# Performance work log

Measured on AMD Instinct MI355X. Metric: run time of the kernel, lower is better.

The kernel has to match this reference:

```python
import jax, jax.numpy as jnp
import numpy as np

B, N, T, F = 8, 5000, 24, 10
H = 128
HEADS = 4
HORIZON = 6
E = 80000
NEG_SLOPE = 0.2


def setup_inputs() -> dict:
    key = jax.random.key(0)
    ks = jax.random.split(key, 24)
    s = 0.1
    inp = {
        'x': jax.random.normal(ks[0], (B, N, T, F), jnp.float32),
        'w_ih0': jax.random.normal(ks[1], (3 * H, F), jnp.float32) * s,
        'w_hh0': jax.random.normal(ks[2], (3 * H, H), jnp.float32) * s,
        'b_ih0': jax.random.normal(ks[3], (3 * H,), jnp.float32) * s,
        'b_hh0': jax.random.normal(ks[4], (3 * H,), jnp.float32) * s,
        'w_ih1': jax.random.normal(ks[5], (3 * H, H), jnp.float32) * s,
        'w_hh1': jax.random.normal(ks[6], (3 * H, H), jnp.float32) * s,
        'b_ih1': jax.random.normal(ks[7], (3 * H,), jnp.float32) * s,
        'b_hh1': jax.random.normal(ks[8], (3 * H,), jnp.float32) * s,
        'gat1_w': jax.random.normal(ks[9], (HEADS * H, H), jnp.float32) * s,
        'gat1_asrc': jax.random.normal(ks[10], (HEADS, H), jnp.float32) * s,
        'gat1_adst': jax.random.normal(ks[11], (HEADS, H), jnp.float32) * s,
        'gat1_b': jax.random.normal(ks[12], (H,), jnp.float32) * s,
        'gat2_w': jax.random.normal(ks[13], (HEADS * H, H), jnp.float32) * s,
        'gat2_asrc': jax.random.normal(ks[14], (HEADS, H), jnp.float32) * s,
        'gat2_adst': jax.random.normal(ks[15], (HEADS, H), jnp.float32) * s,
        'gat2_b': jax.random.normal(ks[16], (H,), jnp.float32) * s,
        'fc_w': jax.random.normal(ks[17], (HORIZON, H), jnp.float32) * s,
        'fc_b': jax.random.normal(ks[18], (HORIZON,), jnp.float32) * s,
        'edge_index': jax.random.randint(ks[19], (2, E), 0, N, jnp.int64),
    }
    return inp


def _gru_layer(xs, w_ih, w_hh, b_ih, b_hh):
    # xs: [BN, T, Fin] -> outputs [BN, T, H] (PyTorch GRU gate order r,z,n)
    gi = jnp.einsum('btf,gf->btg', xs, w_ih) + b_ih  # [BN, T, 3H]
    h0 = jnp.zeros((xs.shape[0], H), xs.dtype)

    def step(h, gi_t):
        gh = h @ w_hh.T + b_hh
        i_r, i_z, i_n = jnp.split(gi_t, 3, axis=-1)
        h_r, h_z, h_n = jnp.split(gh, 3, axis=-1)
        r = jax.nn.sigmoid(i_r + h_r)
        z = jax.nn.sigmoid(i_z + h_z)
        n = jnp.tanh(i_n + r * h_n)
        h_new = (1.0 - z) * n + z * h
        return h_new, h_new

    _, hs = jax.lax.scan(step, h0, jnp.swapaxes(gi, 0, 1))
    return jnp.swapaxes(hs, 0, 1)


def _gat(h, src, dst, W, a_src, a_dst, b, num_nodes):
    # PyG GATConv, heads=4, concat=False (mean), self-loops already in src/dst
    wh = (h @ W.T).reshape(num_nodes, HEADS, H)          # [BN, heads, H]
    alpha_s = jnp.sum(wh * a_src[None], axis=-1)          # [BN, heads]
    alpha_d = jnp.sum(wh * a_dst[None], axis=-1)
    e = jax.nn.leaky_relu(alpha_s[src] + alpha_d[dst], NEG_SLOPE)  # [Eb, heads]
    emax = jax.ops.segment_max(e, dst, num_segments=num_nodes)
    emax = jnp.where(jnp.isfinite(emax), emax, 0.0)
    ex = jnp.exp(e - emax[dst])
    denom = jax.ops.segment_sum(ex, dst, num_segments=num_nodes)
    alpha = ex / (denom[dst] + 1e-16)                     # segment softmax over incoming edges
    out = jax.ops.segment_sum(alpha[..., None] * wh[src], dst, num_segments=num_nodes)
    return out.mean(axis=1) + b


def _batched_edges(edge_index):
    offsets = (jnp.arange(B, dtype=edge_index.dtype) * N)[:, None]
    src = (edge_index[0][None, :] + offsets).reshape(-1)
    dst = (edge_index[1][None, :] + offsets).reshape(-1)
    loops = jnp.arange(B * N, dtype=edge_index.dtype)     # PyG add_self_loops=True
    return jnp.concatenate([src, loops]), jnp.concatenate([dst, loops])


def reference(x, w_ih0, w_hh0, b_ih0, b_hh0, w_ih1, w_hh1, b_ih1, b_hh1,
              gat1_w, gat1_asrc, gat1_adst, gat1_b,
              gat2_w, gat2_asrc, gat2_adst, gat2_b,
              fc_w, fc_b, edge_index):
    src, dst = _batched_edges(edge_index)
    xs = x.reshape(B * N, T, F)
    h1 = _gru_layer(xs, w_ih0, w_hh0, b_ih0, b_hh0)
    h2 = _gru_layer(h1, w_ih1, w_hh1, b_ih1, b_hh1)
    temporal = h2[:, -1, :]                               # [B*N, H]
    s = jax.nn.relu(_gat(temporal, src, dst, gat1_w, gat1_asrc, gat1_adst, gat1_b, B * N))
    s = jax.nn.relu(_gat(s, src, dst, gat2_w, gat2_asrc, gat2_adst, gat2_b, B * N))
    out = s @ fc_w.T + fc_b
    return out.reshape(B, N, HORIZON)
```

## Files before the change

kernel.cpp:

```cpp
#include <hip/hip_runtime.h>
#include <math.h>

#define T_STEPS 24
#define F_IN 10
#define HDIM 128
#define E_EDGES 80000
#define B_BATCH 8
#define N_NODES 5000
#define BN_TOTAL 40000
#define BE 640000
#define NE 680000

typedef __attribute__((ext_vector_type(8))) short s16x8;
typedef __attribute__((ext_vector_type(4))) short s16x4;
typedef __attribute__((ext_vector_type(4))) float fx4;
typedef __attribute__((ext_vector_type(2))) float fx2;
typedef __attribute__((ext_vector_type(4))) unsigned int ux4;
typedef __attribute__((ext_vector_type(2))) unsigned int ux2;

__device__ __forceinline__ float rcpf_(float v) { return __builtin_amdgcn_rcpf(v); }
__device__ __forceinline__ float sigmoidf_(float v) { return rcpf_(1.f + __expf(-v)); }
__device__ __forceinline__ float tanhf_(float v) { float e = __expf(2.f * v); return 1.f - 2.f * rcpf_(e + 1.f); }

__device__ __forceinline__ short f2b(float f) {
    unsigned u = __float_as_uint(f);
    unsigned r = (u + 0x7fffu + ((u >> 16) & 1u)) >> 16;
    return (short)r;
}
__device__ __forceinline__ unsigned int pkbf(float a, float b) {
    unsigned int r;
    asm("v_cvt_pk_bf16_f32 %0, %1, %2" : "=v"(r) : "v"(a), "v"(b));
    return r;
}
__device__ __forceinline__ float bfu(unsigned short u) {
    return __uint_as_float(((unsigned)u) << 16);
}

#define VMW0 asm volatile("s_waitcnt vmcnt(0)" ::: "memory")

__global__ void pack_w(const float* __restrict__ wih0, const float* __restrict__ whh0,
                       const float* __restrict__ wih1, const float* __restrict__ whh1,
                       const float* __restrict__ g1w, const float* __restrict__ g2w,
                       short* __restrict__ pk) {
    int id = blockIdx.x * 256 + threadIdx.x;
    if (id >= 290816) return;
    if (id < 147456) {
        int mat = id / 49152, r = id % 49152;
        int nf = r / 2048, r2 = r % 2048, kf = r2 / 512, r3 = r2 % 512, lane = r3 / 8, j = r3 % 8;
        int n = nf * 16 + (lane & 15), k = kf * 32 + (lane >> 4) * 8 + j;
        const float* src = (mat == 0) ? whh0 : (mat == 1) ? whh1 : wih1;
        pk[id] = f2b(src[n * 128 + k]);
    } else if (id < 159744) {
        int r = id - 147456;
        int nf = r / 512, r2 = r % 512, lane = r2 / 8, j = r2 % 8;
        int n = nf * 16 + (lane & 15), k = (lane >> 4) * 8 + j;
        pk[id] = (k < F_IN) ? f2b(wih0[n * F_IN + k]) : (short)0;
    } else {
        const float* src = (id < 225280) ? g1w : g2w;
        int r = (id < 225280) ? (id - 159744) : (id - 225280);
        int nf = r / 2048, r2 = r % 2048, kf = r2 / 512, r3 = r2 % 512, lane = r3 / 8, j = r3 % 8;
        int n = nf * 16 + (lane & 15), k = kf * 32 + (lane >> 4) * 8 + j;
        pk[id] = f2b(src[n * 128 + k]);
    }
}

__global__ __launch_bounds__(512, 1) void gru_mfma(
    const float* __restrict__ x, const short* __restrict__ pk,
    const float* __restrict__ bih0, const float* __restrict__ bhh0,
    const float* __restrict__ bih1, const float* __restrict__ bhh1,
    float* __restrict__ temporal) {
    __shared__ __align__(16) short h1b[64 * 128];
    __shared__ __align__(16) short h2b[64 * 128];
    __shared__ __align__(16) short ih1s[49152];
    __shared__ __align__(16) short ih0s[12288];
    __shared__ __align__(16) float blds[2][4][128];
    const int tid = threadIdx.x;
    const int w = tid >> 6, l = tid & 63;
    const int lm = l & 15, lk = l >> 4;
    const int jb = w * 16 + lk * 4;
    const long sb = (long)blockIdx.x * 64;

    {
        const char* src1 = (const char*)(pk + 98304);
#pragma unroll
        for (int r = 0; r < 12; ++r) {
            const int off = (w * 12 + r) * 1024;
            __builtin_amdgcn_global_load_lds(
                (const __attribute__((address_space(1))) unsigned int*)(src1 + off + l * 16),
                (__attribute__((address_space(3))) unsigned int*)((char*)ih1s + off), 16, 0, 0);
        }
        const char* src0 = (const char*)(pk + 147456);
#pragma unroll
        for (int r = 0; r < 3; ++r) {
            const int off = (w * 3 + r) * 1024;
            __builtin_amdgcn_global_load_lds(
                (const __attribute__((address_space(1))) unsigned int*)(src0 + off + l * 16),
                (__attribute__((address_space(3))) unsigned int*)((char*)ih0s + off), 16, 0, 0);
        }
    }
    if (tid < 128) {
        const int j = tid;
        blds[0][0][j] = bih0[j] + bhh0[j];
        blds[0][1][j] = bih0[128 + j] + bhh0[128 + j];
        blds[0][2][j] = bhh0[256 + j];
        blds[0][3][j] = bih0[256 + j];
    } else if (tid < 256) {
        const int j = tid - 128;
        blds[1][0][j] = bih1[j] + bhh1[j];
        blds[1][1][j] = bih1[128 + j] + bhh1[128 + j];
        blds[1][2][j] = bhh1[256 + j];
        blds[1][3][j] = bih1[256 + j];
    }
    for (int i = tid; i < 64 * 128; i += 512) { h1b[i] = 0; h2b[i] = 0; }

    s16x8 whh0r[3][4], whh1r[3][4];
#pragma unroll
    for (int g = 0; g < 3; ++g)
#pragma unroll
        for (int kf = 0; kf < 4; ++kf) {
            const int idx = ((((g * 8 + w) * 4) + kf) * 64 + l) * 8;
            whh0r[g][kf] = *(const s16x8*)&pk[idx];
            whh1r[g][kf] = *(const s16x8*)&pk[49152 + idx];
        }

    fx4 h1s[4], h2s[4];
#pragma unroll
    for (int mf = 0; mf < 4; ++mf) { h1s[mf] = (fx4)(0.f); h2s[mf] = (fx4)(0.f); }

    VMW0;
    __syncthreads();

    for (int tt = 0; tt < T_STEPS; ++tt) {
        ux4 xu[4];
#pragma unroll
        for (int mf = 0; mf < 4; ++mf) {
            fx2 a0 = (fx2)(0.f), a1 = (fx2)(0.f), a2 = (fx2)(0.f), a3 = (fx2)(0.f);
            const float* xr = x + (sb + mf * 16 + lm) * (T_STEPS * F_IN) + tt * F_IN;
            if (lk == 0) {
                a0 = *(const fx2*)(xr);     a1 = *(const fx2*)(xr + 2);
                a2 = *(const fx2*)(xr + 4); a3 = *(const fx2*)(xr + 6);
            } else if (lk == 1) {
                a0 = *(const fx2*)(xr + 8);
            }
            ux4 t = { pkbf(a0.x, a0.y), pkbf(a1.x, a1.y), pkbf(a2.x, a2.y), pkbf(a3.x, a3.y) };
            xu[mf] = t;
        }
        fx4 acc[4][4];
#pragma unroll
        for (int p = 0; p < 4; ++p) {
            const fx4 bv = *(const fx4*)&blds[0][p][jb];
#pragma unroll
            for (int mf = 0; mf < 4; ++mf) acc[p][mf] = bv;
        }
#pragma unroll
        for (int kf = 0; kf < 4; ++kf) {
            s16x8 bfr[4];
#pragma unroll
            for (int mf = 0; mf < 4; ++mf) {
                const int m = mf * 16 + lm;
                const int slot = (kf * 4 + lk) ^ (m & 7);
                bfr[mf] = *(const s16x8*)&h1b[m * 128 + slot * 8];
            }
#pragma unroll
            for (int g = 0; g < 3; ++g) {
                const int part = (g == 2) ? 2 : g;
#pragma unroll
                for (int mf = 0; mf < 4; ++mf)
                    acc[part][mf] = __builtin_amdgcn_mfma_f32_16x16x32_bf16(whh0r[g][kf], bfr[mf], acc[part][mf], 0, 0, 0);
            }
        }
#pragma unroll
        for (int g = 0; g < 3; ++g) {
            const int part = (g == 2) ? 3 : g;
            const s16x8 af = *(const s16x8*)&ih0s[((g * 8 + w) * 64 + l) * 8];
#pragma unroll
            for (int mf = 0; mf < 4; ++mf)
                acc[part][mf] = __builtin_amdgcn_mfma_f32_16x16x32_bf16(af, __builtin_bit_cast(s16x8, xu[mf]), acc[part][mf], 0, 0, 0);
        }
        ux2 w1[4];
#pragma unroll
        for (int mf = 0; mf < 4; ++mf) {
#pragma unroll
            for (int rg = 0; rg < 4; ++rg) {
                const float r = sigmoidf_(acc[0][mf][rg]);
                const float z = sigmoidf_(acc[1][mf][rg]);
                const float n = tanhf_(acc[3][mf][rg] + r * acc[2][mf][rg]);
                h1s[mf][rg] = n + z * (h1s[mf][rg] - n);
            }
            ux2 q = { pkbf(h1s[mf][0], h1s[mf][1]), pkbf(h1s[mf][2], h1s[mf][3]) };
            w1[mf] = q;
        }
#pragma unroll
        for (int p = 0; p < 4; ++p) {
            const fx4 bv = *(const fx4*)&blds[1][p][jb];
#pragma unroll
            for (int mf = 0; mf < 4; ++mf) acc[p][mf] = bv;
        }
#pragma unroll
        for (int kf = 0; kf < 4; ++kf) {
            s16x8 bfr[4];
#pragma unroll
            for (int mf = 0; mf < 4; ++mf) {
                const int m = mf * 16 + lm;
                const int slot = (kf * 4 + lk) ^ (m & 7);
                bfr[mf] = *(const s16x8*)&h2b[m * 128 + slot * 8];
            }
#pragma unroll
            for (int g = 0; g < 3; ++g) {
                const int part = (g == 2) ? 2 : g;
#pragma unroll
                for (int mf = 0; mf < 4; ++mf)
                    acc[part][mf] = __builtin_amdgcn_mfma_f32_16x16x32_bf16(whh1r[g][kf], bfr[mf], acc[part][mf], 0, 0, 0);
            }
        }
        __syncthreads();
#pragma unroll
        for (int mf = 0; mf < 4; ++mf) {
            const int m = mf * 16 + lm;
            const int slot = (jb >> 3) ^ (m & 7);
            *(ux2*)&h1b[m * 128 + slot * 8 + (jb & 7)] = w1[mf];
        }
        __syncthreads();
#pragma unroll
        for (int kf = 0; kf < 4; ++kf) {
            s16x8 bfr[4];
#pragma unroll
            for (int mf = 0; mf < 4; ++mf) {
                const int m = mf * 16 + lm;
                const int slot = (kf * 4 + lk) ^ (m & 7);
                bfr[mf] = *(const s16x8*)&h1b[m * 128 + slot * 8];
            }
#pragma unroll
            for (int g = 0; g < 3; ++g) {
                const int part = (g == 2) ? 3 : g;
                const s16x8 af = *(const s16x8*)&ih1s[((((g * 8 + w) * 4) + kf) * 64 + l) * 8];
#pragma unroll
                for (int mf = 0; mf < 4; ++mf)
                    acc[part][mf] = __builtin_amdgcn_mfma_f32_16x16x32_bf16(af, bfr[mf], acc[part][mf], 0, 0, 0);
            }
        }
#pragma unroll
        for (int mf = 0; mf < 4; ++mf) {
#pragma unroll
            for (int rg = 0; rg < 4; ++rg) {
                const float r = sigmoidf_(acc[0][mf][rg]);
                const float z = sigmoidf_(acc[1][mf][rg]);
                const float n = tanhf_(acc[3][mf][rg] + r * acc[2][mf][rg]);
                h2s[mf][rg] = n + z * (h2s[mf][rg] - n);
            }
            const int m = mf * 16 + lm;
            const int slot = (jb >> 3) ^ (m & 7);
            ux2 q = { pkbf(h2s[mf][0], h2s[mf][1]), pkbf(h2s[mf][2], h2s[mf][3]) };
            *(ux2*)&h2b[m * 128 + slot * 8 + (jb & 7)] = q;
        }
        __syncthreads();
    }
#pragma unroll
    for (int mf = 0; mf < 4; ++mf) {
        const long m = sb + mf * 16 + lm;
        *(fx4*)&temporal[m * 128 + jb] = h2s[mf];
    }
}

__global__ void csr_count(const int* __restrict__ edge1, int* __restrict__ cnt) {
    int e = blockIdx.x * 256 + threadIdx.x;
    if (e >= NE) return;
    int d;
    if (e < BE) { int b = e / E_EDGES; d = edge1[e - b * E_EDGES] + b * N_NODES; }
    else d = e - BE;
    atomicAdd(&cnt[d], 1);
}

__global__ void csr_scan(const int* cnt, int* offs, int* curs) {
    __shared__ int part[1024];
    const int t = threadIdx.x;
    const int base = t * 40;
    int end = base + 40; if (end > BN_TOTAL) end = BN_TOTAL;
    int s = 0;
    for (int i = base; i < end; ++i) s += cnt[i];
    part[t] = s;
    __syncthreads();
    for (int off = 1; off < 1024; off <<= 1) {
        int v = (t >= off) ? part[t - off] : 0;
        __syncthreads();
        part[t] += v;
        __syncthreads();
    }
    int run = part[t] - s;
    for (int i = base; i < end; ++i) {
        int c = cnt[i];
        offs[i] = run; curs[i] = run; run += c;
    }
    if (t == 1023) offs[BN_TOTAL] = NE;
}

__global__ void csr_fill(const int* __restrict__ edge1, int* __restrict__ curs, int* __restrict__ esort) {
    int e = blockIdx.x * 256 + threadIdx.x;
    if (e >= NE) return;
    int d;
    if (e < BE) { int b = e / E_EDGES; d = edge1[e - b * E_EDGES] + b * N_NODES; }
    else d = e - BE;
    int pos = atomicAdd(&curs[d], 1);
    esort[pos] = e;
}

__global__ __launch_bounds__(256, 2) void gat_gemm(const float* __restrict__ feat,
                                                   const short* __restrict__ pkg,
                                                   const float* __restrict__ asrc,
                                                   const float* __restrict__ adst,
                                                   unsigned short* __restrict__ whb,
                                                   float* __restrict__ AS, float* __restrict__ AD) {
    __shared__ __align__(16) short fb[128 * 128];
    __shared__ float reda[4][128];
    __shared__ float redb[4][128];
    const int tid = threadIdx.x;
    const int w = tid >> 6, l = tid & 63;
    const int lm = l & 15, lk = l >> 4;
    const int i0 = blockIdx.x * 128;
    const int j0 = blockIdx.y * 128;
#pragma unroll
    for (int it = 0; it < 16; ++it) {
        const int idx = it * 256 + tid;
        const int r = idx >> 5, kq = idx & 31;
        fx4 v = (fx4)(0.f);
        const int row = i0 + r;
        if (row < BN_TOTAL) v = *(const fx4*)&feat[(size_t)row * 128 + kq * 4];
        const int slot = (kq >> 1) ^ (r & 7);
        ux2 pv = { pkbf(v.x, v.y), pkbf(v.z, v.w) };
        *(ux2*)&fb[r * 128 + slot * 8 + (kq & 1) * 4] = pv;
    }
    __syncthreads();
    fx4 acc[2][8];
#pragma unroll
    for (int jf = 0; jf < 2; ++jf)
#pragma unroll
        for (int mf = 0; mf < 8; ++mf) acc[jf][mf] = (fx4)(0.f);
#pragma unroll
    for (int kf = 0; kf < 4; ++kf) {
        s16x8 bfr[8];
#pragma unroll
        for (int mf = 0; mf < 8; ++mf) {
            const int m = mf * 16 + lm;
            const int slot = (kf * 4 + lk) ^ (m & 7);
            bfr[mf] = *(const s16x8*)&fb[m * 128 + slot * 8];
        }
#pragma unroll
        for (int jf = 0; jf < 2; ++jf) {
            const int nf = (j0 >> 4) + w * 2 + jf;
            const s16x8 af = *(const s16x8*)&pkg[((nf * 4 + kf) * 64 + l) * 8];
#pragma unroll
            for (int mf = 0; mf < 8; ++mf)
                acc[jf][mf] = __builtin_amdgcn_mfma_f32_16x16x32_bf16(af, bfr[mf], acc[jf][mf], 0, 0, 0);
        }
    }
    float ps[8], pd[8];
#pragma unroll
    for (int mf = 0; mf < 8; ++mf) { ps[mf] = 0.f; pd[mf] = 0.f; }
#pragma unroll
    for (int jf = 0; jf < 2; ++jf) {
        const int cb = w * 32 + jf * 16 + lk * 4;
        const fx4 s4 = *(const fx4*)&asrc[j0 + cb];
        const fx4 d4 = *(const fx4*)&adst[j0 + cb];
        const int nb = j0 + cb;
#pragma unroll
        for (int mf = 0; mf < 8; ++mf) {
            const int m = i0 + mf * 16 + lm;
            const fx4 a = acc[jf][mf];
            if (m < BN_TOTAL) {
                ux2 pv = { pkbf(a.x, a.y), pkbf(a.z, a.w) };
                *(ux2*)&whb[(size_t)m * 512 + nb] = pv;
            }
            ps[mf] += a.x * s4.x + a.y * s4.y + a.z * s4.z + a.w * s4.w;
            pd[mf] += a.x * d4.x + a.y * d4.y + a.z * d4.z + a.w * d4.w;
        }
    }
#pragma unroll
    for (int off = 16; off <= 32; off <<= 1) {
#pragma unroll
        for (int mf = 0; mf < 8; ++mf) {
            ps[mf] += __shfl_xor(ps[mf], off);
            pd[mf] += __shfl_xor(pd[mf], off);
        }
    }
    if (lk == 0) {
#pragma unroll
        for (int mf = 0; mf < 8; ++mf) {
            reda[w][mf * 16 + lm] = ps[mf];
            redb[w][mf * 16 + lm] = pd[mf];
        }
    }
    __syncthreads();
    if (tid < 128) {
        const int row = i0 + tid;
        if (row < BN_TOTAL) {
            const float a = reda[0][tid] + reda[1][tid] + reda[2][tid] + reda[3][tid];
            const float b = redb[0][tid] + redb[1][tid] + redb[2][tid] + redb[3][tid];
            AS[row * 4 + (j0 >> 7)] = a;
            AD[row * 4 + (j0 >> 7)] = b;
        }
    }
}

__device__ __forceinline__ int decode_src(int eid, const int* __restrict__ edge0) {
    if (eid < BE) { int b = eid / E_EDGES; return edge0[eid - b * E_EDGES] + b * N_NODES; }
    return eid - BE;
}

__global__ __launch_bounds__(256) void gat_aggregate(const unsigned short* __restrict__ whb,
                                                     const float* __restrict__ AS, const float* __restrict__ AD,
                                                     const int* __restrict__ offs, const int* __restrict__ esort,
                                                     const int* __restrict__ edge0, const float* __restrict__ bias,
                                                     float* __restrict__ outf,
                                                     const float* __restrict__ fcw, const float* __restrict__ fcb,
                                                     float* __restrict__ out6) {
    const int lane = threadIdx.x & 63;
    const int bid = blockIdx.x;
    const int d = (bid & 7) * N_NODES + (bid >> 3) * 4 + (threadIdx.x >> 6);
    const int e0 = offs[d], e1 = offs[d + 1];
    const fx4 ad4 = *(const fx4*)&AD[d * 4];
    float mx0 = -1e30f, mx1 = -1e30f, mx2 = -1e30f, mx3 = -1e30f;
    float den0 = 0.f, den1 = 0.f, den2 = 0.f, den3 = 0.f;
    float acc[8] = {0.f, 0.f, 0.f, 0.f, 0.f, 0.f, 0.f, 0.f};
    for (int e = e0; e < e1; ++e) {
        const int src = decode_src(esort[e], edge0);
        const fx4 as4 = *(const fx4*)&AS[src * 4];
        float v0 = as4.x + ad4.x; v0 = v0 > 0.f ? v0 : 0.2f * v0;
        float v1 = as4.y + ad4.y; v1 = v1 > 0.f ? v1 : 0.2f * v1;
        float v2 = as4.z + ad4.z; v2 = v2 > 0.f ? v2 : 0.2f * v2;
        float v3 = as4.w + ad4.w; v3 = v3 > 0.f ? v3 : 0.2f * v3;
        const float n0 = fmaxf(mx0, v0), n1 = fmaxf(mx1, v1), n2 = fmaxf(mx2, v2), n3 = fmaxf(mx3, v3);
        const float c0 = __expf(mx0 - n0), c1 = __expf(mx1 - n1), c2 = __expf(mx2 - n2), c3 = __expf(mx3 - n3);
        const float ex0 = __expf(v0 - n0), ex1 = __expf(v1 - n1), ex2 = __expf(v2 - n2), ex3 = __expf(v3 - n3);
        mx0 = n0; mx1 = n1; mx2 = n2; mx3 = n3;
        den0 = den0 * c0 + ex0; den1 = den1 * c1 + ex1;
        den2 = den2 * c2 + ex2; den3 = den3 * c3 + ex3;
        const unsigned int* wr = (const unsigned int*)(whb + (size_t)src * 512);
        const unsigned int u0 = wr[lane];
        const unsigned int u1 = wr[64 + lane];
        const unsigned int u2 = wr[128 + lane];
        const unsigned int u3 = wr[192 + lane];
        acc[0] = acc[0] * c0 + ex0 * bfu((unsigned short)u0);
        acc[1] = acc[1] * c0 + ex0 * bfu((unsigned short)(u0 >> 16));
        acc[2] = acc[2] * c1 + ex1 * bfu((unsigned short)u1);
        acc[3] = acc[3] * c1 + ex1 * bfu((unsigned short)(u1 >> 16));
        acc[4] = acc[4] * c2 + ex2 * bfu((unsigned short)u2);
        acc[5] = acc[5] * c2 + ex2 * bfu((unsigned short)(u2 >> 16));
        acc[6] = acc[6] * c3 + ex3 * bfu((unsigned short)u3);
        acc[7] = acc[7] * c3 + ex3 * bfu((unsigned short)(u3 >> 16));
    }
    const float i0v = rcpf_(den0 + 1e-16f), i1v = rcpf_(den1 + 1e-16f);
    const float i2v = rcpf_(den2 + 1e-16f), i3v = rcpf_(den3 + 1e-16f);
    const int c0i = 2 * lane, c1i = 2 * lane + 1;
    const float o0r = 0.25f * (acc[0] * i0v + acc[2] * i1v + acc[4] * i2v + acc[6] * i3v) + bias[c0i];
    const float o1r = 0.25f * (acc[1] * i0v + acc[3] * i1v + acc[5] * i2v + acc[7] * i3v) + bias[c1i];
    const float o0 = fmaxf(o0r, 0.f);
    const float o1 = fmaxf(o1r, 0.f);
    if (fcw == nullptr) {
        fx2 ov = { o0, o1 };
        *(fx2*)&outf[(size_t)d * 128 + c0i] = ov;
    } else {
        float p[6];
#pragma unroll
        for (int m = 0; m < 6; ++m) p[m] = o0 * fcw[m * 128 + c0i] + o1 * fcw[m * 128 + c1i];
#pragma unroll
        for (int off = 32; off > 0; off >>= 1) {
#pragma unroll
            for (int m = 0; m < 6; ++m) p[m] += __shfl_down(p[m], off);
        }
        if (lane == 0) {
#pragma unroll
            for (int m = 0; m < 6; ++m) out6[(size_t)d * 6 + m] = p[m] + fcb[m];
        }
    }
}

extern "C" void kernel_launch(void* const* d_in, const int* in_sizes, int n_in,
                              void* d_out, int out_size, void* d_ws, size_t ws_size,
                              hipStream_t stream) {
    const float* x = (const float*)d_in[0];
    const float* wih0 = (const float*)d_in[1];
    const float* whh0 = (const float*)d_in[2];
    const float* bih0 = (const float*)d_in[3];
    const float* bhh0 = (const float*)d_in[4];
    const float* wih1 = (const float*)d_in[5];
    const float* whh1 = (const float*)d_in[6];
    const float* bih1 = (const float*)d_in[7];
    const float* bhh1 = (const float*)d_in[8];
    const float* g1w = (const float*)d_in[9];
    const float* g1as = (const float*)d_in[10];
    const float* g1ad = (const float*)d_in[11];
    const float* g1b = (const float*)d_in[12];
    const float* g2w = (const float*)d_in[13];
    const float* g2as = (const float*)d_in[14];
    const float* g2ad = (const float*)d_in[15];
    const float* g2b = (const float*)d_in[16];
    const float* fcw = (const float*)d_in[17];
    const float* fcb = (const float*)d_in[18];
    const int* eidx = (const int*)d_in[19];
    const int* edge0 = eidx;
    const int* edge1 = eidx + E_EDGES;

    char* ws = (char*)d_ws;
    float* H0 = (float*)ws;
    float* H1 = (float*)(ws + 20480000);
    unsigned short* WHB = (unsigned short*)(ws + 40960000);
    float* AS = (float*)(ws + 122880000);
    float* AD = (float*)(ws + 123520000);
    short* PK = (short*)(ws + 124160000);
    int* OFFS = (int*)(ws + 124765184);
    int* CURS = (int*)(ws + 124925248);
    int* ESORT = (int*)(ws + 125085248);

    hipMemsetAsync(CURS, 0, BN_TOTAL * sizeof(int), stream);
    pack_w<<<1136, 256, 0, stream>>>(wih0, whh0, wih1, whh1, g1w, g2w, PK);
    csr_count<<<(NE + 255) / 256, 256, 0, stream>>>(edge1, CURS);
    csr_scan<<<1, 1024, 0, stream>>>(CURS, OFFS, CURS);
    csr_fill<<<(NE + 255) / 256, 256, 0, stream>>>(edge1, CURS, ESORT);

    gru_mfma<<<625, 512, 0, stream>>>(x, PK, bih0, bhh0, bih1, bhh1, H0);

    dim3 gg(313, 4);
    gat_gemm<<<gg, 256, 0, stream>>>(H0, PK + 159744, g1as, g1ad, WHB, AS, AD);
    gat_aggregate<<<10000, 256, 0, stream>>>(WHB, AS, AD, OFFS, ESORT, edge0, g1b, H1,
                                             nullptr, nullptr, nullptr);

    gat_gemm<<<gg, 256, 0, stream>>>(H1, PK + 225280, g2as, g2ad, WHB, AS, AD);
    gat_aggregate<<<10000, 256, 0, stream>>>(WHB, AS, AD, OFFS, ESORT, edge0, g2b, nullptr,
                                             fcw, fcb, (float*)d_out);
}
```

Measured before the change: 1.047 ms.

## Shrink GRU tiles for occupancy and drop online-softmax max in GAT aggregate

```diff
diff --git a/kernel.cpp b/kernel.cpp
--- a/kernel.cpp
+++ b/kernel.cpp
@@ -35,8 +35,6 @@
 __device__ __forceinline__ float bfu(unsigned short u) {
     return __uint_as_float(((unsigned)u) << 16);
 }
-
-#define VMW0 asm volatile("s_waitcnt vmcnt(0)" ::: "memory")
 
 __global__ void pack_w(const float* __restrict__ wih0, const float* __restrict__ whh0,
                        const float* __restrict__ wih1, const float* __restrict__ whh1,
@@ -64,40 +62,20 @@
     }
 }
 
-__global__ __launch_bounds__(512, 1) void gru_mfma(
+__global__ __launch_bounds__(512, 4) void gru_mfma(
     const float* __restrict__ x, const short* __restrict__ pk,
     const float* __restrict__ bih0, const float* __restrict__ bhh0,
     const float* __restrict__ bih1, const float* __restrict__ bhh1,
     float* __restrict__ temporal) {
-    __shared__ __align__(16) short h1b[64 * 128];
-    __shared__ __align__(16) short h2b[64 * 128];
-    __shared__ __align__(16) short ih1s[49152];
-    __shared__ __align__(16) short ih0s[12288];
+    __shared__ __align__(16) short h1b[32 * 128];
+    __shared__ __align__(16) short h2b[32 * 128];
     __shared__ __align__(16) float blds[2][4][128];
     const int tid = threadIdx.x;
     const int w = tid >> 6, l = tid & 63;
     const int lm = l & 15, lk = l >> 4;
     const int jb = w * 16 + lk * 4;
-    const long sb = (long)blockIdx.x * 64;
-
-    {
-        const char* src1 = (const char*)(pk + 98304);
-#pragma unroll
-        for (int r = 0; r < 12; ++r) {
-            const int off = (w * 12 + r) * 1024;
-            __builtin_amdgcn_global_load_lds(
-                (const __attribute__((address_space(1))) unsigned int*)(src1 + off + l * 16),
-                (__attribute__((address_space(3))) unsigned int*)((char*)ih1s + off), 16, 0, 0);
-        }
-        const char* src0 = (const char*)(pk + 147456);
-#pragma unroll
-        for (int r = 0; r < 3; ++r) {
-            const int off = (w * 3 + r) * 1024;
-            __builtin_amdgcn_global_load_lds(
-                (const __attribute__((address_space(1))) unsigned int*)(src0 + off + l * 16),
-                (__attribute__((address_space(3))) unsigned int*)((char*)ih0s + off), 16, 0, 0);
-        }
-    }
+    const long sb = (long)blockIdx.x * 32;
+
     if (tid < 128) {
         const int j = tid;
         blds[0][0][j] = bih0[j] + bhh0[j];
@@ -111,29 +89,18 @@
         blds[1][2][j] = bhh1[256 + j];
         blds[1][3][j] = bih1[256 + j];
     }
-    for (int i = tid; i < 64 * 128; i += 512) { h1b[i] = 0; h2b[i] = 0; }
-
-    s16x8 whh0r[3][4], whh1r[3][4];
-#pragma unroll
-    for (int g = 0; g < 3; ++g)
-#pragma unroll
-        for (int kf = 0; kf < 4; ++kf) {
-            const int idx = ((((g * 8 + w) * 4) + kf) * 64 + l) * 8;
-            whh0r[g][kf] = *(const s16x8*)&pk[idx];
-            whh1r[g][kf] = *(const s16x8*)&pk[49152 + idx];
-        }
-
-    fx4 h1s[4], h2s[4];
-#pragma unroll
-    for (int mf = 0; mf < 4; ++mf) { h1s[mf] = (fx4)(0.f); h2s[mf] = (fx4)(0.f); }
-
-    VMW0;
+    for (int i = tid; i < 32 * 128; i += 512) { h1b[i] = 0; h2b[i] = 0; }
+
+    fx4 h1s[2], h2s[2];
+#pragma unroll
+    for (int mf = 0; mf < 2; ++mf) { h1s[mf] = (fx4)(0.f); h2s[mf] = (fx4)(0.f); }
+
     __syncthreads();
 
     for (int tt = 0; tt < T_STEPS; ++tt) {
-        ux4 xu[4];
-#pragma unroll
-        for (int mf = 0; mf < 4; ++mf) {
+        ux4 xu[2];
+#pragma unroll
+        for (int mf = 0; mf < 2; ++mf) {
             fx2 a0 = (fx2)(0.f), a1 = (fx2)(0.f), a2 = (fx2)(0.f), a3 = (fx2)(0.f);
             const float* xr = x + (sb + mf * 16 + lm) * (T_STEPS * F_IN) + tt * F_IN;
             if (lk == 0) {
@@ -145,18 +112,17 @@
             ux4 t = { pkbf(a0.x, a0.y), pkbf(a1.x, a1.y), pkbf(a2.x, a2.y), pkbf(a3.x, a3.y) };
             xu[mf] = t;
         }
-        fx4 acc[4][4];
+        fx4 acc[4][2];
 #pragma unroll
         for (int p = 0; p < 4; ++p) {
             const fx4 bv = *(const fx4*)&blds[0][p][jb];
-#pragma unroll
-            for (int mf = 0; mf < 4; ++mf) acc[p][mf] = bv;
+            acc[p][0] = bv; acc[p][1] = bv;
         }
 #pragma unroll
         for (int kf = 0; kf < 4; ++kf) {
-            s16x8 bfr[4];
-#pragma unroll
-            for (int mf = 0; mf < 4; ++mf) {
+            s16x8 bfr[2];
+#pragma unroll
+            for (int mf = 0; mf < 2; ++mf) {
                 const int m = mf * 16 + lm;
                 const int slot = (kf * 4 + lk) ^ (m & 7);
                 bfr[mf] = *(const s16x8*)&h1b[m * 128 + slot * 8];
@@ -164,22 +130,23 @@
 #pragma unroll
             for (int g = 0; g < 3; ++g) {
                 const int part = (g == 2) ? 2 : g;
-#pragma unroll
-                for (int mf = 0; mf < 4; ++mf)
-                    acc[part][mf] = __builtin_amdgcn_mfma_f32_16x16x32_bf16(whh0r[g][kf], bfr[mf], acc[part][mf], 0, 0, 0);
+                const s16x8 af = *(const s16x8*)&pk[((((g * 8 + w) * 4) + kf) * 64 + l) * 8];
+#pragma unroll
+                for (int mf = 0; mf < 2; ++mf)
+                    acc[part][mf] = __builtin_amdgcn_mfma_f32_16x16x32_bf16(af, bfr[mf], acc[part][mf], 0, 0, 0);
             }
         }
 #pragma unroll
         for (int g = 0; g < 3; ++g) {
             const int part = (g == 2) ? 3 : g;
-            const s16x8 af = *(const s16x8*)&ih0s[((g * 8 + w) * 64 + l) * 8];
-#pragma unroll
-            for (int mf = 0; mf < 4; ++mf)
+            const s16x8 af = *(const s16x8*)&pk[147456 + ((g * 8 + w) * 64 + l) * 8];
+#pragma unroll
+            for (int mf = 0; mf < 2; ++mf)
                 acc[part][mf] = __builtin_amdgcn_mfma_f32_16x16x32_bf16(af, __builtin_bit_cast(s16x8, xu[mf]), acc[part][mf], 0, 0, 0);
         }
-        ux2 w1[4];
-#pragma unroll
-        for (int mf = 0; mf < 4; ++mf) {
+        ux2 w1[2];
+#pragma unroll
+        for (int mf = 0; mf < 2; ++mf) {
 #pragma unroll
             for (int rg = 0; rg < 4; ++rg) {
                 const float r = sigmoidf_(acc[0][mf][rg]);
@@ -193,14 +160,13 @@
 #pragma unroll
         for (int p = 0; p < 4; ++p) {
             const fx4 bv = *(const fx4*)&blds[1][p][jb];
-#pragma unroll
-            for (int mf = 0; mf < 4; ++mf) acc[p][mf] = bv;
+            acc[p][0] = bv; acc[p][1] = bv;
         }
 #pragma unroll
         for (int kf = 0; kf < 4; ++kf) {
-            s16x8 bfr[4];
-#pragma unroll
-            for (int mf = 0; mf < 4; ++mf) {
+            s16x8 bfr[2];
+#pragma unroll
+            for (int mf = 0; mf < 2; ++mf) {
                 const int m = mf * 16 + lm;
                 const int slot = (kf * 4 + lk) ^ (m & 7);
                 bfr[mf] = *(const s16x8*)&h2b[m * 128 + slot * 8];
@@ -208,14 +174,15 @@
 #pragma unroll
             for (int g = 0; g < 3; ++g) {
                 const int part = (g == 2) ? 2 : g;
-#pragma unroll
-                for (int mf = 0; mf < 4; ++mf)
-                    acc[part][mf] = __builtin_amdgcn_mfma_f32_16x16x32_bf16(whh1r[g][kf], bfr[mf], acc[part][mf], 0, 0, 0);
+                const s16x8 af = *(const s16x8*)&pk[49152 + ((((g * 8 + w) * 4) + kf) * 64 + l) * 8];
+#pragma unroll
+                for (int mf = 0; mf < 2; ++mf)
+                    acc[part][mf] = __builtin_amdgcn_mfma_f32_16x16x32_bf16(af, bfr[mf], acc[part][mf], 0, 0, 0);
             }
         }
         __syncthreads();
 #pragma unroll
-        for (int mf = 0; mf < 4; ++mf) {
+        for (int mf = 0; mf < 2; ++mf) {
             const int m = mf * 16 + lm;
             const int slot = (jb >> 3) ^ (m & 7);
             *(ux2*)&h1b[m * 128 + slot * 8 + (jb & 7)] = w1[mf];
@@ -223,9 +190,9 @@
         __syncthreads();
 #pragma unroll
         for (int kf = 0; kf < 4; ++kf) {
-            s16x8 bfr[4];
-#pragma unroll
-            for (int mf = 0; mf < 4; ++mf) {
+            s16x8 bfr[2];
+#pragma unroll
+            for (int mf = 0; mf < 2; ++mf) {
                 const int m = mf * 16 + lm;
                 const int slot = (kf * 4 + lk) ^ (m & 7);
                 bfr[mf] = *(const s16x8*)&h1b[m * 128 + slot * 8];
@@ -233,14 +200,14 @@
 #pragma unroll
             for (int g = 0; g < 3; ++g) {
                 const int part = (g == 2) ? 3 : g;
-                const s16x8 af = *(const s16x8*)&ih1s[((((g * 8 + w) * 4) + kf) * 64 + l) * 8];
-#pragma unroll
-                for (int mf = 0; mf < 4; ++mf)
+                const s16x8 af = *(const s16x8*)&pk[98304 + ((((g * 8 + w) * 4) + kf) * 64 + l) * 8];
+#pragma unroll
+                for (int mf = 0; mf < 2; ++mf)
                     acc[part][mf] = __builtin_amdgcn_mfma_f32_16x16x32_bf16(af, bfr[mf], acc[part][mf], 0, 0, 0);
             }
         }
 #pragma unroll
-        for (int mf = 0; mf < 4; ++mf) {
+        for (int mf = 0; mf < 2; ++mf) {
 #pragma unroll
             for (int rg = 0; rg < 4; ++rg) {
                 const float r = sigmoidf_(acc[0][mf][rg]);
@@ -256,7 +223,7 @@
         __syncthreads();
     }
 #pragma unroll
-    for (int mf = 0; mf < 4; ++mf) {
+    for (int mf = 0; mf < 2; ++mf) {
         const long m = sb + mf * 16 + lm;
         *(fx4*)&temporal[m * 128 + jb] = h2s[mf];
     }
@@ -418,7 +385,6 @@
     const int d = (bid & 7) * N_NODES + (bid >> 3) * 4 + (threadIdx.x >> 6);
     const int e0 = offs[d], e1 = offs[d + 1];
     const fx4 ad4 = *(const fx4*)&AD[d * 4];
-    float mx0 = -1e30f, mx1 = -1e30f, mx2 = -1e30f, mx3 = -1e30f;
     float den0 = 0.f, den1 = 0.f, den2 = 0.f, den3 = 0.f;
     float acc[8] = {0.f, 0.f, 0.f, 0.f, 0.f, 0.f, 0.f, 0.f};
     for (int e = e0; e < e1; ++e) {
@@ -428,25 +394,21 @@
         float v1 = as4.y + ad4.y; v1 = v1 > 0.f ? v1 : 0.2f * v1;
         float v2 = as4.z + ad4.z; v2 = v2 > 0.f ? v2 : 0.2f * v2;
         float v3 = as4.w + ad4.w; v3 = v3 > 0.f ? v3 : 0.2f * v3;
-        const float n0 = fmaxf(mx0, v0), n1 = fmaxf(mx1, v1), n2 = fmaxf(mx2, v2), n3 = fmaxf(mx3, v3);
-        const float c0 = __expf(mx0 - n0), c1 = __expf(mx1 - n1), c2 = __expf(mx2 - n2), c3 = __expf(mx3 - n3);
-        const float ex0 = __expf(v0 - n0), ex1 = __expf(v1 - n1), ex2 = __expf(v2 - n2), ex3 = __expf(v3 - n3);
-        mx0 = n0; mx1 = n1; mx2 = n2; mx3 = n3;
-        den0 = den0 * c0 + ex0; den1 = den1 * c1 + ex1;
-        den2 = den2 * c2 + ex2; den3 = den3 * c3 + ex3;
+        const float ex0 = __expf(v0), ex1 = __expf(v1), ex2 = __expf(v2), ex3 = __expf(v3);
+        den0 += ex0; den1 += ex1; den2 += ex2; den3 += ex3;
         const unsigned int* wr = (const unsigned int*)(whb + (size_t)src * 512);
         const unsigned int u0 = wr[lane];
         const unsigned int u1 = wr[64 + lane];
         const unsigned int u2 = wr[128 + lane];
         const unsigned int u3 = wr[192 + lane];
-        acc[0] = acc[0] * c0 + ex0 * bfu((unsigned short)u0);
-        acc[1] = acc[1] * c0 + ex0 * bfu((unsigned short)(u0 >> 16));
-        acc[2] = acc[2] * c1 + ex1 * bfu((unsigned short)u1);
-        acc[3] = acc[3] * c1 + ex1 * bfu((unsigned short)(u1 >> 16));
-        acc[4] = acc[4] * c2 + ex2 * bfu((unsigned short)u2);
-        acc[5] = acc[5] * c2 + ex2 * bfu((unsigned short)(u2 >> 16));
-        acc[6] = acc[6] * c3 + ex3 * bfu((unsigned short)u3);
-        acc[7] = acc[7] * c3 + ex3 * bfu((unsigned short)(u3 >> 16));
+        acc[0] += ex0 * bfu((unsigned short)u0);
+        acc[1] += ex0 * bfu((unsigned short)(u0 >> 16));
+        acc[2] += ex1 * bfu((unsigned short)u1);
+        acc[3] += ex1 * bfu((unsigned short)(u1 >> 16));
+        acc[4] += ex2 * bfu((unsigned short)u2);
+        acc[5] += ex2 * bfu((unsigned short)(u2 >> 16));
+        acc[6] += ex3 * bfu((unsigned short)u3);
+        acc[7] += ex3 * bfu((unsigned short)(u3 >> 16));
     }
     const float i0v = rcpf_(den0 + 1e-16f), i1v = rcpf_(den1 + 1e-16f);
     const float i2v = rcpf_(den2 + 1e-16f), i3v = rcpf_(den3 + 1e-16f);
@@ -517,7 +479,7 @@
     csr_scan<<<1, 1024, 0, stream>>>(CURS, OFFS, CURS);
     csr_fill<<<(NE + 255) / 256, 256, 0, stream>>>(edge1, CURS, ESORT);
 
-    gru_mfma<<<625, 512, 0, stream>>>(x, PK, bih0, bhh0, bih1, bhh1, H0);
+    gru_mfma<<<1250, 512, 0, stream>>>(x, PK, bih0, bhh0, bih1, bhh1, H0);
 
     dim3 gg(313, 4);
     gat_gemm<<<gg, 256, 0, stream>>>(H0, PK + 159744, g1as, g1ad, WHB, AS, AD);
```

Result: slower. 1.462 ms (+39.6%).
